# Optimization experiments

Hardware: AMD Instinct MI355X
Metric: run time of the kernel (lower is better)

Reference implementation:

```python
import jax, jax.numpy as jnp
import numpy as np

NUM_GROUPS = 8
EPS = 1e-5


def group_norm(x, gamma, beta):
    # x: [B, C, H, W], groups over channel dim
    b, c, h, w = x.shape
    xg = x.reshape(b, NUM_GROUPS, c // NUM_GROUPS, h, w)
    mean = xg.mean(axis=(2, 3, 4), keepdims=True)
    var = xg.var(axis=(2, 3, 4), keepdims=True)
    xg = (xg - mean) * jax.lax.rsqrt(var + EPS)
    x = xg.reshape(b, c, h, w)
    return x * gamma[None, :, None, None] + beta[None, :, None, None]


def conv1x1(x, w, bias):
    # 1x1 conv == per-pixel linear: [B,C,H,W] x [O,C] -> [B,O,H,W]
    return jnp.einsum('bchw,oc->bohw', x, w) + bias[None, :, None, None]


def setup_inputs() -> dict:
    key = jax.random.key(0)
    ks = jax.random.split(key, 6)
    B, C, H, W = 16, 512, 32, 32
    s = 1.0 / np.sqrt(C)  # conv2d default init scale-ish
    return {
        'x': jax.random.normal(ks[0], (B, C, H, W), jnp.float32),
        'gn_w': jnp.ones((C,), jnp.float32),
        'gn_b': jnp.zeros((C,), jnp.float32),
        'wq': jax.random.normal(ks[1], (C, C), jnp.float32) * s,
        'bq': jnp.zeros((C,), jnp.float32),
        'wk': jax.random.normal(ks[2], (C, C), jnp.float32) * s,
        'bk': jnp.zeros((C,), jnp.float32),
        'wv': jax.random.normal(ks[3], (C, C), jnp.float32) * s,
        'bv': jnp.zeros((C,), jnp.float32),
        'wo': jax.random.normal(ks[4], (C, C), jnp.float32) * s,
        'bo': jnp.zeros((C,), jnp.float32),
    }


def reference(x, gn_w, gn_b, wq, bq, wk, bk, wv, bv, wo, bo):
    b, c, h, w = x.shape
    scale = c ** (-0.5)
    hn = group_norm(x, gn_w, gn_b)
    q = conv1x1(hn, wq, bq).reshape(b, c, h * w).transpose(0, 2, 1)  # [B, N, C]
    k = conv1x1(hn, wk, bk).reshape(b, c, h * w).transpose(0, 2, 1)  # [B, N, C]
    v = conv1x1(hn, wv, bv).reshape(b, c, h * w).transpose(0, 2, 1)  # [B, N, C]
    attn = jnp.einsum('bnc,bmc->bnm', q, k) * scale                 # [B, N, N]
    attn = jax.nn.softmax(attn, axis=-1)
    out = jnp.einsum('bnm,bmc->bnc', attn, v)                       # [B, N, C]
    out = out.transpose(0, 2, 1).reshape(b, c, h, w)
    out = conv1x1(out, wo, bo)
    return x + out
```

## Files before the change

### kernel.cpp

```cpp
#include <hip/hip_runtime.h>
#include <stdint.h>

#define C_DIM 512
#define HW_N  1024
#define CPG   64
#define EPS_GN 1e-5f
#define SCALE_QK 0.044194173824159216f

typedef __attribute__((ext_vector_type(8))) __bf16 bf16x8v;
typedef __attribute__((ext_vector_type(4))) float  f32x4;

typedef __attribute__((address_space(1))) void gvoid_t;
typedef __attribute__((address_space(3))) void lvoid_t;

constexpr long long SNC = (long long)HW_N * C_DIM;
constexpr long long SNN = (long long)HW_N * 1024;

__device__ __forceinline__ void gload_lds16(const void* g, void* l) {
  __builtin_amdgcn_global_load_lds((gvoid_t*)g, (lvoid_t*)l, 16, 0, 0);
}

__device__ __forceinline__ uint16_t f2bfbits(float f) {
  __bf16 h = (__bf16)f;
  return __builtin_bit_cast(uint16_t, h);
}

__device__ __forceinline__ float bf2f(uint16_t u) {
  return __builtin_bit_cast(float, (uint32_t)u << 16);
}

template<int N>
__device__ __forceinline__ void vm_wait() {
  if constexpr (N == 0)      asm volatile("s_waitcnt vmcnt(0)" ::: "memory");
  else if constexpr (N == 2) asm volatile("s_waitcnt vmcnt(2)" ::: "memory");
  else if constexpr (N == 3) asm volatile("s_waitcnt vmcnt(3)" ::: "memory");
  else                       asm volatile("s_waitcnt vmcnt(6)" ::: "memory");
}

struct BlkId { int bx, by, bz; };
__device__ __forceinline__ BlkId xcd_decode(int gx, int gy) {
  const int nwg = gridDim.x;
  const int bid = blockIdx.x;
  const int wg  = (bid & 7) * (nwg >> 3) + (bid >> 3);
  const int pb  = gx * gy;
  const int bz  = wg / pb;
  const int rem = wg - bz * pb;
  const int by  = rem / gx;
  const int bx  = rem - by * gx;
  return {bx, by, bz};
}

__global__ __launch_bounds__(256)
void prep_stats_kernel(const float* __restrict__ wq, const float* __restrict__ wk,
                       const float* __restrict__ wv, const float* __restrict__ wo,
                       const float* __restrict__ bq, const float* __restrict__ bk,
                       const float* __restrict__ x,
                       __bf16* __restrict__ wqkb, __bf16* __restrict__ wvb,
                       __bf16* __restrict__ wob, float* __restrict__ bqk,
                       float2* __restrict__ part)
{
  const int blk = blockIdx.x;
  const int t = threadIdx.x;
  if (blk < 1024) {
    const int which = blk >> 8;
    const int i = (blk & 255) * 256 + t;
    const float* src = (which == 0) ? wq : (which == 1) ? wk : (which == 2) ? wv : wo;
    __bf16* dst = (which == 0) ? wqkb
               : (which == 1) ? (wqkb + (size_t)C_DIM * C_DIM)
               : (which == 2) ? wvb : wob;
    const float scale = (which == 0) ? SCALE_QK : 1.f;
    float4 v = ((const float4*)src)[i];
    uint32_t lo = (uint32_t)f2bfbits(v.x * scale) | ((uint32_t)f2bfbits(v.y * scale) << 16);
    uint32_t hi = (uint32_t)f2bfbits(v.z * scale) | ((uint32_t)f2bfbits(v.w * scale) << 16);
    ((uint2*)dst)[i] = make_uint2(lo, hi);
  } else if (blk == 1024) {
    for (int j = t; j < 1024; j += 256)
      bqk[j] = (j < 512) ? bq[j] * SCALE_QK : bk[j - 512];
  } else {
    const int lin  = blk - 1025;
    const int b    = lin >> 4;
    const int g    = (lin >> 1) & 7;
    const int half = lin & 1;
    const float4* xv = (const float4*)(x + ((long long)(b * C_DIM + g * CPG)) * HW_N
                                         + half * 512);
    float s1 = 0.f, s2 = 0.f;
    for (int i = t; i < 64 * 128; i += 256) {
      const int c  = i >> 7;
      const int nf = i & 127;
      float4 v = xv[c * 256 + nf];
      s1 += v.x + v.y + v.z + v.w;
      s2 += v.x * v.x + v.y * v.y + v.z * v.z + v.w * v.w;
    }
    #pragma unroll
    for (int off = 32; off; off >>= 1) {
      s1 += __shfl_xor(s1, off);
      s2 += __shfl_xor(s2, off);
    }
    __shared__ float red[2][4];
    const int w = t >> 6, l = t & 63;
    if (l == 0) { red[0][w] = s1; red[1][w] = s2; }
    __syncthreads();
    if (t == 0) {
      s1 = red[0][0] + red[0][1] + red[0][2] + red[0][3];
      s2 = red[1][0] + red[1][1] + red[1][2] + red[1][3];
      part[lin] = make_float2(s1, s2);
    }
  }
}

__global__ __launch_bounds__(512)
void gn_norm(const float* __restrict__ x, const float2* __restrict__ part,
             const float* __restrict__ gnw, const float* __restrict__ gnb,
             __bf16* __restrict__ hn)
{
  const int b  = blockIdx.x >> 4;
  const int nc = blockIdx.x & 15;
  const int t  = threadIdx.x;

  __shared__ float asc[512], bsc[512];
  __shared__ float tile[64][65];

  {
    const int c = t;
    const int g = c >> 6;
    float2 p0 = part[(b * 8 + g) * 2 + 0];
    float2 p1 = part[(b * 8 + g) * 2 + 1];
    const float mean = (p0.x + p1.x) * (1.f / 65536.f);
    const float var  = (p0.y + p1.y) * (1.f / 65536.f) - mean * mean;
    const float rstd = rsqrtf(var + EPS_GN);
    const float a = rstd * gnw[c];
    asc[c] = a;
    bsc[c] = gnb[c] - mean * a;
  }
  __syncthreads();

  const long long xb = (long long)b * C_DIM * HW_N + nc * 64;
  __bf16* ob = hn + ((long long)b * HW_N + nc * 64) * C_DIM;

  for (int cg = 0; cg < 8; ++cg) {
    #pragma unroll
    for (int pass = 0; pass < 2; ++pass) {
      const int task = pass * 512 + t;
      const int c  = task >> 4;
      const int f4 = task & 15;
      float4 v = *(const float4*)(x + xb + (long long)(cg * 64 + c) * HW_N + f4 * 4);
      const float a  = asc[cg * 64 + c];
      const float bb = bsc[cg * 64 + c];
      tile[c][f4 * 4 + 0] = v.x * a + bb;
      tile[c][f4 * 4 + 1] = v.y * a + bb;
      tile[c][f4 * 4 + 2] = v.z * a + bb;
      tile[c][f4 * 4 + 3] = v.w * a + bb;
    }
    __syncthreads();
    {
      const int n  = t >> 3;
      const int gc = t & 7;
      uint32_t p[4];
      #pragma unroll
      for (int j = 0; j < 4; ++j) {
        const float f0 = tile[gc * 8 + 2 * j + 0][n];
        const float f1 = tile[gc * 8 + 2 * j + 1][n];
        p[j] = (uint32_t)f2bfbits(f0) | ((uint32_t)f2bfbits(f1) << 16);
      }
      *(uint4*)(ob + (long long)n * C_DIM + cg * 64 + gc * 8) =
          make_uint4(p[0], p[1], p[2], p[3]);
    }
    __syncthreads();
  }
}

__global__ __launch_bounds__(256)
void softmax_kernel(__bf16* __restrict__ S)
{
  const long long row = blockIdx.x;
  uint2* sp = (uint2*)(S + row * HW_N);
  const int t = threadIdx.x;
  uint2 raw = sp[t];
  float v0 = bf2f((uint16_t)(raw.x & 0xffff));
  float v1 = bf2f((uint16_t)(raw.x >> 16));
  float v2 = bf2f((uint16_t)(raw.y & 0xffff));
  float v3 = bf2f((uint16_t)(raw.y >> 16));
  float m = fmaxf(fmaxf(v0, v1), fmaxf(v2, v3));
  #pragma unroll
  for (int off = 32; off; off >>= 1) m = fmaxf(m, __shfl_xor(m, off));
  __shared__ float redm[4];
  __shared__ float reds[4];
  const int w = t >> 6, l = t & 63;
  if (l == 0) redm[w] = m;
  __syncthreads();
  m = fmaxf(fmaxf(redm[0], redm[1]), fmaxf(redm[2], redm[3]));
  float e0 = __expf(v0 - m), e1 = __expf(v1 - m);
  float e2 = __expf(v2 - m), e3 = __expf(v3 - m);
  float sum = e0 + e1 + e2 + e3;
  #pragma unroll
  for (int off = 32; off; off >>= 1) sum += __shfl_xor(sum, off);
  if (l == 0) reds[w] = sum;
  __syncthreads();
  sum = reds[0] + reds[1] + reds[2] + reds[3];
  const float inv = 1.f / sum;
  uint32_t lo = (uint32_t)f2bfbits(e0 * inv) | ((uint32_t)f2bfbits(e1 * inv) << 16);
  uint32_t hi = (uint32_t)f2bfbits(e2 * inv) | ((uint32_t)f2bfbits(e3 * inv) << 16);
  sp[t] = make_uint2(lo, hi);
}

template<int BN, int OUTM, int BIASM>
__device__ __forceinline__ void gemm_body(char* lds,
    const __bf16* __restrict__ Ab, const __bf16* __restrict__ Bb,
    void* __restrict__ Cb, const float* __restrict__ bias,
    const float* __restrict__ resid,
    int lda, int ldb, int ldc, int K, int m0, int n0)
{
  constexpr int CB = BN / 128;
  constexpr int CH = 1 + CB;
  constexpr int NF = BN / 64;
  constexpr int TILE_B = 8192 * CH;

  const int tt = threadIdx.x;
  const int w  = tt >> 6;
  const int l  = tt & 63;
  const int lr = l & 15;
  const int lg = l >> 4;
  const int wm = w >> 2;
  const int wn = w & 3;

  const int srow = tt >> 2;
  const int sgr  = (tt & 3) ^ ((tt >> 3) & 3);

  f32x4 acc[4][NF];
  #pragma unroll
  for (int f = 0; f < 4; ++f)
    #pragma unroll
    for (int c = 0; c < NF; ++c)
      acc[f][c] = (f32x4){0.f, 0.f, 0.f, 0.f};

  auto stage = [&](int t, int c) {
    char* dst = lds + (t % 3) * TILE_B + c * 8192 + w * 1024;
    const __bf16* src = (c == 0)
      ? Ab + (long long)(m0 + srow) * lda + (t << 5) + sgr * 8
      : Bb + (long long)(n0 + (c - 1) * 128 + srow) * ldb + (t << 5) + sgr * 8;
    gload_lds16(src, dst);
  };
  auto rdA = [&](const char* base, int f) -> bf16x8v {
    const int row = wm * 64 + f * 16 + lr;
    return *(const bf16x8v*)(base + row * 64 + ((lg ^ ((row >> 1) & 3)) << 4));
  };
  auto rdB = [&](const char* base, int c) -> bf16x8v {
    const int row = wn * (BN / 4) + c * 16 + lr;
    return *(const bf16x8v*)(base + 8192 + row * 64 + ((lg ^ ((row >> 1) & 3)) << 4));
  };

  const int NT = K >> 5;

  #pragma unroll
  for (int c = 0; c < CH; ++c) stage(0, c);
  #pragma unroll
  for (int c = 0; c < CH; ++c) stage(1, c);
  vm_wait<CH>();
  __builtin_amdgcn_s_barrier();
  __builtin_amdgcn_sched_barrier(0);

  for (int t = 0; t < NT; ++t) {
    const char* buf = lds + (t % 3) * TILE_B;

    if (t + 2 < NT) {
      #pragma unroll
      for (int c = 0; c < CH; ++c) stage(t + 2, c);
    }
    bf16x8v Bf[NF], Af[4];
    #pragma unroll
    for (int c = 0; c < NF; ++c) Bf[c] = rdB(buf, c);
    #pragma unroll
    for (int f = 0; f < 4; ++f)  Af[f] = rdA(buf, f);
    #pragma unroll
    for (int f = 0; f < 4; ++f)
      #pragma unroll
      for (int c = 0; c < NF; ++c)
        acc[f][c] = __builtin_amdgcn_mfma_f32_16x16x32_bf16(Af[f], Bf[c], acc[f][c], 0, 0, 0);
    __builtin_amdgcn_sched_barrier(0);
    if (t + 2 < NT) vm_wait<CH>();
    else            vm_wait<0>();
    __builtin_amdgcn_s_barrier();
    __builtin_amdgcn_sched_barrier(0);
  }

  #pragma unroll
  for (int f = 0; f < 4; ++f) {
    const int rrb = m0 + wm * 64 + f * 16 + lg * 4;
    #pragma unroll
    for (int c = 0; c < NF; ++c) {
      const int cc = n0 + wn * (BN / 4) + c * 16 + lr;
      const float cbias = (BIASM == 1) ? bias[cc] : 0.f;
      #pragma unroll
      for (int r = 0; r < 4; ++r) {
        const int rr = rrb + r;
        float v = acc[f][c][r];
        if (BIASM == 1) v += cbias;
        if (BIASM == 2) v += bias[rr];
        const long long idx = (long long)rr * ldc + cc;
        if (OUTM == 0) {
          ((__bf16*)Cb)[idx] = (__bf16)v;
        } else if (OUTM == 2) {
          ((float*)Cb)[idx] = v;
        } else {
          ((float*)Cb)[idx] = v + resid[idx];
        }
      }
    }
  }
}

__global__ __launch_bounds__(512, 4)
void qkv_kernel(const __bf16* __restrict__ hn, const __bf16* __restrict__ wqkb,
                const __bf16* __restrict__ wvb,
                __bf16* __restrict__ qkb, __bf16* __restrict__ vtb,
                const float* __restrict__ bqk, const float* __restrict__ bv)
{
  __shared__ alignas(16) char lds[73728];
  const int wg = (blockIdx.x & 7) * 96 + (blockIdx.x >> 3);
  if (wg < 512) {
    const int bz = wg >> 5, rem = wg & 31, by = rem >> 2, bx = rem & 3;
    gemm_body<256, 0, 1>(lds, hn + (long long)bz * SNC, wqkb,
                         (void*)(qkb + (long long)bz * SNN), bqk, nullptr,
                         C_DIM, C_DIM, 1024, C_DIM, by * 128, bx * 256);
  } else {
    const int wg2 = wg - 512;
    const int bz = wg2 >> 4, rem = wg2 & 15, by = rem >> 2, bx = rem & 3;
    gemm_body<256, 0, 2>(lds, wvb, hn + (long long)bz * SNC,
                         (void*)(vtb + (long long)bz * SNC), bv, nullptr,
                         C_DIM, C_DIM, HW_N, C_DIM, by * 128, bx * 256);
  }
}

template<int BN, int OUTM, int BIASM>
__global__ __launch_bounds__(512, 4)
void gemm8k(const __bf16* __restrict__ A, const __bf16* __restrict__ B,
            void* __restrict__ C, const float* __restrict__ bias,
            const float* __restrict__ resid,
            int lda, int ldb, int ldc,
            long long aS, long long bS, long long cS, int K, int gx, int gy)
{
  __shared__ alignas(16) char lds[8192 * (1 + BN / 128) * 3];
  const BlkId id = xcd_decode(gx, gy);
  const __bf16* Ab = A + (long long)id.bz * aS;
  const __bf16* Bb = B + (long long)id.bz * bS;
  void* Cb = (OUTM == 0) ? (void*)((__bf16*)C + (long long)id.bz * cS)
                         : (void*)((float*)C + (long long)id.bz * cS);
  const float* rb = (OUTM == 1) ? (resid + (long long)id.bz * cS) : nullptr;
  gemm_body<BN, OUTM, BIASM>(lds, Ab, Bb, Cb, bias, rb,
                             lda, ldb, ldc, K, id.by * 128, id.bx * BN);
}

extern "C" void kernel_launch(void* const* d_in, const int* in_sizes, int n_in,
                              void* d_out, int out_size, void* d_ws, size_t ws_size,
                              hipStream_t stream)
{
  const float* x   = (const float*)d_in[0];
  const float* gnw = (const float*)d_in[1];
  const float* gnb = (const float*)d_in[2];
  const float* wq  = (const float*)d_in[3];
  const float* bq  = (const float*)d_in[4];
  const float* wk  = (const float*)d_in[5];
  const float* bk  = (const float*)d_in[6];
  const float* wv  = (const float*)d_in[7];
  const float* bv  = (const float*)d_in[8];
  const float* wo  = (const float*)d_in[9];
  const float* bo  = (const float*)d_in[10];
  (void)in_sizes; (void)n_in; (void)out_size; (void)ws_size;

  size_t used = 0;
  char* base = (char*)d_ws;
  auto carve = [&](size_t bytes) -> void* {
    used = (used + 255) & ~(size_t)255;
    void* p = base + used;
    used += bytes;
    return p;
  };

  __bf16* wqkb = (__bf16*)carve((size_t)2 * C_DIM * C_DIM * 2);
  __bf16* wvb  = (__bf16*)carve((size_t)C_DIM * C_DIM * 2);
  __bf16* wob  = (__bf16*)carve((size_t)C_DIM * C_DIM * 2);
  float*  bqk  = (float*) carve((size_t)1024 * 4);
  float2* part = (float2*)carve((size_t)256 * 8);

  __bf16* hn   = (__bf16*)carve((size_t)16 * HW_N * C_DIM * 2);
  __bf16* qkb  = (__bf16*)carve((size_t)16 * HW_N * 1024 * 2);
  __bf16* vtb  = (__bf16*)carve((size_t)16 * C_DIM * HW_N * 2);
  __bf16* o1b  = (__bf16*)carve((size_t)16 * HW_N * C_DIM * 2);
  __bf16* Sb   = (__bf16*)carve((size_t)16 * HW_N * HW_N * 2);

  prep_stats_kernel<<<dim3(1281), 256, 0, stream>>>(wq, wk, wv, wo, bq, bk, x,
                                                    wqkb, wvb, wob, bqk, part);
  gn_norm<<<dim3(256), 512, 0, stream>>>(x, part, gnw, gnb, hn);

  qkv_kernel<<<dim3(768), 512, 0, stream>>>(hn, wqkb, wvb, qkb, vtb, bqk, bv);

  gemm8k<256, 0, 0><<<dim3(512), 512, 0, stream>>>(qkb, qkb + 512, Sb,
      nullptr, nullptr, 1024, 1024, 1024, SNN, SNN, SNN, C_DIM, 4, 8);

  softmax_kernel<<<dim3(16 * 1024), 256, 0, stream>>>(Sb);

  gemm8k<128, 0, 0><<<dim3(512), 512, 0, stream>>>(Sb, vtb, o1b,
      nullptr, nullptr, 1024, 1024, C_DIM, SNN, SNC, SNC, HW_N, 4, 8);

  gemm8k<128, 1, 2><<<dim3(512), 512, 0, stream>>>(wob, o1b, (void*)d_out,
      bo, x, C_DIM, C_DIM, HW_N, 0, SNC, SNC, C_DIM, 8, 4);
}
```

Baseline: 139.2 us.

## Unify GEMMs on 128x128 tile with 4 waves and 4x4 MFMA fragments per wave

Replaces the 8-wave 128xBN GEMM body with a single 256-thread 128x128 tile kernel in which each wave computes a 64x64 sub-tile (4x4 MFMA fragments). The QKV and QK^T launches go from 256-wide tiles to 128-wide tiles with doubled grid sizes. The aim is higher per-wave MFMA density and more LDS reuse per fragment load, with more blocks resident per CU. The cost is more accumulator registers per wave and more A-tile reloads for the formerly 256-wide GEMMs.

```diff
diff --git a/kernel.cpp b/kernel.cpp
--- a/kernel.cpp
+++ b/kernel.cpp
@@ -31,10 +31,16 @@
 
 template<int N>
 __device__ __forceinline__ void vm_wait() {
-  if constexpr (N == 0)      asm volatile("s_waitcnt vmcnt(0)" ::: "memory");
-  else if constexpr (N == 2) asm volatile("s_waitcnt vmcnt(2)" ::: "memory");
-  else if constexpr (N == 3) asm volatile("s_waitcnt vmcnt(3)" ::: "memory");
-  else                       asm volatile("s_waitcnt vmcnt(6)" ::: "memory");
+  static_assert(N >= 0 && N <= 8, "vm_wait: unsupported count");
+  if constexpr (N == 0) asm volatile("s_waitcnt vmcnt(0)" ::: "memory");
+  if constexpr (N == 1) asm volatile("s_waitcnt vmcnt(1)" ::: "memory");
+  if constexpr (N == 2) asm volatile("s_waitcnt vmcnt(2)" ::: "memory");
+  if constexpr (N == 3) asm volatile("s_waitcnt vmcnt(3)" ::: "memory");
+  if constexpr (N == 4) asm volatile("s_waitcnt vmcnt(4)" ::: "memory");
+  if constexpr (N == 5) asm volatile("s_waitcnt vmcnt(5)" ::: "memory");
+  if constexpr (N == 6) asm volatile("s_waitcnt vmcnt(6)" ::: "memory");
+  if constexpr (N == 7) asm volatile("s_waitcnt vmcnt(7)" ::: "memory");
+  if constexpr (N == 8) asm volatile("s_waitcnt vmcnt(8)" ::: "memory");
 }
 
 struct BlkId { int bx, by, bz; };
@@ -203,41 +209,39 @@
   sp[t] = make_uint2(lo, hi);
 }
 
-template<int BN, int OUTM, int BIASM>
-__device__ __forceinline__ void gemm_body(char* lds,
+template<int OUTM, int BIASM>
+__device__ __forceinline__ void gemm128(char* lds,
     const __bf16* __restrict__ Ab, const __bf16* __restrict__ Bb,
     void* __restrict__ Cb, const float* __restrict__ bias,
     const float* __restrict__ resid,
     int lda, int ldb, int ldc, int K, int m0, int n0)
 {
-  constexpr int CB = BN / 128;
-  constexpr int CH = 1 + CB;
-  constexpr int NF = BN / 64;
-  constexpr int TILE_B = 8192 * CH;
+  constexpr int SLOT = 16384;
+  constexpr int CH   = 4;
 
   const int tt = threadIdx.x;
   const int w  = tt >> 6;
   const int l  = tt & 63;
   const int lr = l & 15;
   const int lg = l >> 4;
-  const int wm = w >> 2;
-  const int wn = w & 3;
+  const int wm = w >> 1;
+  const int wn = w & 1;
 
   const int srow = tt >> 2;
   const int sgr  = (tt & 3) ^ ((tt >> 3) & 3);
 
-  f32x4 acc[4][NF];
+  f32x4 acc[4][4];
   #pragma unroll
   for (int f = 0; f < 4; ++f)
     #pragma unroll
-    for (int c = 0; c < NF; ++c)
+    for (int c = 0; c < 4; ++c)
       acc[f][c] = (f32x4){0.f, 0.f, 0.f, 0.f};
 
   auto stage = [&](int t, int c) {
-    char* dst = lds + (t % 3) * TILE_B + c * 8192 + w * 1024;
-    const __bf16* src = (c == 0)
-      ? Ab + (long long)(m0 + srow) * lda + (t << 5) + sgr * 8
-      : Bb + (long long)(n0 + (c - 1) * 128 + srow) * ldb + (t << 5) + sgr * 8;
+    char* dst = lds + (t % 3) * SLOT + c * 4096 + w * 1024;
+    const __bf16* src = (c < 2)
+      ? Ab + (long long)(m0 + c * 64 + srow) * lda + (t << 5) + sgr * 8
+      : Bb + (long long)(n0 + (c - 2) * 64 + srow) * ldb + (t << 5) + sgr * 8;
     gload_lds16(src, dst);
   };
   auto rdA = [&](const char* base, int f) -> bf16x8v {
@@ -245,7 +249,7 @@
     return *(const bf16x8v*)(base + row * 64 + ((lg ^ ((row >> 1) & 3)) << 4));
   };
   auto rdB = [&](const char* base, int c) -> bf16x8v {
-    const int row = wn * (BN / 4) + c * 16 + lr;
+    const int row = wn * 64 + c * 16 + lr;
     return *(const bf16x8v*)(base + 8192 + row * 64 + ((lg ^ ((row >> 1) & 3)) << 4));
   };
 
@@ -260,21 +264,21 @@
   __builtin_amdgcn_sched_barrier(0);
 
   for (int t = 0; t < NT; ++t) {
-    const char* buf = lds + (t % 3) * TILE_B;
+    const char* buf = lds + (t % 3) * SLOT;
 
     if (t + 2 < NT) {
       #pragma unroll
       for (int c = 0; c < CH; ++c) stage(t + 2, c);
     }
-    bf16x8v Bf[NF], Af[4];
-    #pragma unroll
-    for (int c = 0; c < NF; ++c) Bf[c] = rdB(buf, c);
-    #pragma unroll
-    for (int f = 0; f < 4; ++f)  Af[f] = rdA(buf, f);
+    bf16x8v Bf[4], Af[4];
+    #pragma unroll
+    for (int c = 0; c < 4; ++c) Bf[c] = rdB(buf, c);
+    #pragma unroll
+    for (int f = 0; f < 4; ++f) Af[f] = rdA(buf, f);
     #pragma unroll
     for (int f = 0; f < 4; ++f)
       #pragma unroll
-      for (int c = 0; c < NF; ++c)
+      for (int c = 0; c < 4; ++c)
         acc[f][c] = __builtin_amdgcn_mfma_f32_16x16x32_bf16(Af[f], Bf[c], acc[f][c], 0, 0, 0);
     __builtin_amdgcn_sched_barrier(0);
     if (t + 2 < NT) vm_wait<CH>();
@@ -287,8 +291,8 @@
   for (int f = 0; f < 4; ++f) {
     const int rrb = m0 + wm * 64 + f * 16 + lg * 4;
     #pragma unroll
-    for (int c = 0; c < NF; ++c) {
-      const int cc = n0 + wn * (BN / 4) + c * 16 + lr;
+    for (int c = 0; c < 4; ++c) {
+      const int cc = n0 + wn * 64 + c * 16 + lr;
       const float cbias = (BIASM == 1) ? bias[cc] : 0.f;
       #pragma unroll
       for (int r = 0; r < 4; ++r) {
@@ -309,45 +313,45 @@
   }
 }
 
-__global__ __launch_bounds__(512, 4)
+__global__ __launch_bounds__(256, 2)
 void qkv_kernel(const __bf16* __restrict__ hn, const __bf16* __restrict__ wqkb,
                 const __bf16* __restrict__ wvb,
                 __bf16* __restrict__ qkb, __bf16* __restrict__ vtb,
                 const float* __restrict__ bqk, const float* __restrict__ bv)
 {
-  __shared__ alignas(16) char lds[73728];
-  const int wg = (blockIdx.x & 7) * 96 + (blockIdx.x >> 3);
-  if (wg < 512) {
-    const int bz = wg >> 5, rem = wg & 31, by = rem >> 2, bx = rem & 3;
-    gemm_body<256, 0, 1>(lds, hn + (long long)bz * SNC, wqkb,
-                         (void*)(qkb + (long long)bz * SNN), bqk, nullptr,
-                         C_DIM, C_DIM, 1024, C_DIM, by * 128, bx * 256);
+  __shared__ alignas(16) char lds[49152];
+  const int wg = (blockIdx.x & 7) * 192 + (blockIdx.x >> 3);
+  if (wg < 1024) {
+    const int bz = wg >> 6, rem = wg & 63, by = rem >> 3, bx = rem & 7;
+    gemm128<0, 1>(lds, hn + (long long)bz * SNC, wqkb,
+                  (void*)(qkb + (long long)bz * SNN), bqk, nullptr,
+                  C_DIM, C_DIM, 1024, C_DIM, by * 128, bx * 128);
   } else {
-    const int wg2 = wg - 512;
-    const int bz = wg2 >> 4, rem = wg2 & 15, by = rem >> 2, bx = rem & 3;
-    gemm_body<256, 0, 2>(lds, wvb, hn + (long long)bz * SNC,
-                         (void*)(vtb + (long long)bz * SNC), bv, nullptr,
-                         C_DIM, C_DIM, HW_N, C_DIM, by * 128, bx * 256);
-  }
-}
-
-template<int BN, int OUTM, int BIASM>
-__global__ __launch_bounds__(512, 4)
-void gemm8k(const __bf16* __restrict__ A, const __bf16* __restrict__ B,
-            void* __restrict__ C, const float* __restrict__ bias,
-            const float* __restrict__ resid,
-            int lda, int ldb, int ldc,
-            long long aS, long long bS, long long cS, int K, int gx, int gy)
-{
-  __shared__ alignas(16) char lds[8192 * (1 + BN / 128) * 3];
+    const int wg2 = wg - 1024;
+    const int bz = wg2 >> 5, rem = wg2 & 31, by = rem >> 3, bx = rem & 7;
+    gemm128<0, 2>(lds, wvb, hn + (long long)bz * SNC,
+                  (void*)(vtb + (long long)bz * SNC), bv, nullptr,
+                  C_DIM, C_DIM, HW_N, C_DIM, by * 128, bx * 128);
+  }
+}
+
+template<int OUTM, int BIASM>
+__global__ __launch_bounds__(256, 2)
+void gemm128k(const __bf16* __restrict__ A, const __bf16* __restrict__ B,
+              void* __restrict__ C, const float* __restrict__ bias,
+              const float* __restrict__ resid,
+              int lda, int ldb, int ldc,
+              long long aS, long long bS, long long cS, int K, int gx, int gy)
+{
+  __shared__ alignas(16) char lds[49152];
   const BlkId id = xcd_decode(gx, gy);
   const __bf16* Ab = A + (long long)id.bz * aS;
   const __bf16* Bb = B + (long long)id.bz * bS;
   void* Cb = (OUTM == 0) ? (void*)((__bf16*)C + (long long)id.bz * cS)
                          : (void*)((float*)C + (long long)id.bz * cS);
   const float* rb = (OUTM == 1) ? (resid + (long long)id.bz * cS) : nullptr;
-  gemm_body<BN, OUTM, BIASM>(lds, Ab, Bb, Cb, bias, rb,
-                             lda, ldb, ldc, K, id.by * 128, id.bx * BN);
+  gemm128<OUTM, BIASM>(lds, Ab, Bb, Cb, bias, rb,
+                       lda, ldb, ldc, K, id.by * 128, id.bx * 128);
 }
 
 extern "C" void kernel_launch(void* const* d_in, const int* in_sizes, int n_in,
@@ -392,16 +396,16 @@
                                                     wqkb, wvb, wob, bqk, part);
   gn_norm<<<dim3(256), 512, 0, stream>>>(x, part, gnw, gnb, hn);
 
-  qkv_kernel<<<dim3(768), 512, 0, stream>>>(hn, wqkb, wvb, qkb, vtb, bqk, bv);
-
-  gemm8k<256, 0, 0><<<dim3(512), 512, 0, stream>>>(qkb, qkb + 512, Sb,
-      nullptr, nullptr, 1024, 1024, 1024, SNN, SNN, SNN, C_DIM, 4, 8);
+  qkv_kernel<<<dim3(1536), 256, 0, stream>>>(hn, wqkb, wvb, qkb, vtb, bqk, bv);
+
+  gemm128k<0, 0><<<dim3(1024), 256, 0, stream>>>(qkb, qkb + 512, Sb,
+      nullptr, nullptr, 1024, 1024, 1024, SNN, SNN, SNN, C_DIM, 8, 8);
 
   softmax_kernel<<<dim3(16 * 1024), 256, 0, stream>>>(Sb);
 
-  gemm8k<128, 0, 0><<<dim3(512), 512, 0, stream>>>(Sb, vtb, o1b,
+  gemm128k<0, 0><<<dim3(512), 256, 0, stream>>>(Sb, vtb, o1b,
       nullptr, nullptr, 1024, 1024, C_DIM, SNN, SNC, SNC, HW_N, 4, 8);
 
-  gemm8k<128, 1, 2><<<dim3(512), 512, 0, stream>>>(wob, o1b, (void*)d_out,
+  gemm128k<1, 2><<<dim3(512), 256, 0, stream>>>(wob, o1b, (void*)d_out,
       bo, x, C_DIM, C_DIM, HW_N, 0, SNC, SNC, C_DIM, 8, 4);
 }
```

Result: no change. 141.7 us (+1.8%).
